# Optimization experiments

Hardware: AMD Instinct MI355X
Metric: run time of the kernel (lower is better)

## Reference

```python
import jax, jax.numpy as jnp
import numpy as np

S, B, D_MODEL, H = 2048, 2, 1024, 16
DH = D_MODEL // H
SCALE = 1.0 / np.sqrt(DH)
NEG_INF = jnp.float32(-1e30)


def setup_inputs() -> dict:
    key = jax.random.key(0)
    ks = jax.random.split(key, 12)
    std = 1.0 / np.sqrt(D_MODEL)
    inp = {
        "query": jax.random.normal(ks[0], (S, B, D_MODEL), jnp.float32),
        "key": jax.random.normal(ks[1], (S, B, D_MODEL), jnp.float32),
        "value": jax.random.normal(ks[2], (S, B, D_MODEL), jnp.float32),
        # causal mask, shape (seq_q, seq_k, 1) per prepare_mask asserts
        "mask": jnp.tril(jnp.ones((S, S), dtype=bool))[:, :, None],
        # params stored (in, out) for x @ W
        "Wq": jax.random.normal(ks[3], (D_MODEL, H * DH), jnp.float32) * std,
        "bq": jnp.zeros((H * DH,), jnp.float32),
        "Wk": jax.random.normal(ks[4], (D_MODEL, H * DH), jnp.float32) * std,
        "bk": jnp.zeros((H * DH,), jnp.float32),
        "Wv": jax.random.normal(ks[5], (D_MODEL, H * DH), jnp.float32) * std,
        "bv": jnp.zeros((H * DH,), jnp.float32),
        "Wo": jax.random.normal(ks[6], (D_MODEL, D_MODEL), jnp.float32) * std,
        "bo": jnp.zeros((D_MODEL,), jnp.float32),
    }
    return inp


def reference(query, key, value, mask, Wq, bq, Wk, bk, Wv, bv, Wo, bo):
    seq_len, batch, _ = query.shape
    # project and split heads: (S, B, H, DH)
    q = (query @ Wq + bq).reshape(seq_len, batch, H, DH)
    k = (key @ Wk + bk).reshape(key.shape[0], batch, H, DH)
    v = (value @ Wv + bv).reshape(value.shape[0], batch, H, DH)
    # scores: (seq_q, batch, heads, seq_k)
    scores = jnp.einsum("ibhd,jbhd->ibhj", q, k) * SCALE
    # mask (seq_q, seq_k, batch_or_1) -> broadcast to (seq_q, batch, 1, seq_k)
    m = jnp.transpose(mask, (0, 2, 1))[:, :, None, :]
    scores = jnp.where(m, scores, NEG_INF)
    attn = jax.nn.softmax(scores, axis=-1)  # dropout_prob=0.0 (eval)
    x = jnp.einsum("ibhj,jbhd->ibhd", attn, v)
    x = x.reshape(seq_len, batch, H * DH)
    return x @ Wo + bo
```

## Files before the change

### kernel.cpp

```cpp
#include <hip/hip_runtime.h>
#include <hip/hip_bf16.h>
#include <cstdint>

#define S_LEN 2048
#define BATCH 2
#define DM    1024
#define NH    16
#define DH    64
#define SL2E  0.18033688011112042f

typedef short s8v __attribute__((ext_vector_type(8)));
typedef float f4v __attribute__((ext_vector_type(4)));

__device__ __forceinline__ ushort f2bf(float x) {
  union { float f; uint32_t u; } v; v.f = x;
  uint32_t r = v.u + 0x7fffu + ((v.u >> 16) & 1u);
  return (ushort)(r >> 16);
}

typedef __attribute__((address_space(1))) const void gas_void;
typedef __attribute__((address_space(3))) void las_void;
__device__ __forceinline__ void gld16(void* l, const void* g) {
  __builtin_amdgcn_global_load_lds((gas_void*)(uintptr_t)g,
                                   (las_void*)(uintptr_t)l, 16, 0, 0);
}

__global__ __launch_bounds__(256)
void wtrans(const float* W0, const float* W1, const float* W2, const float* W3,
            ushort* T0, ushort* T1, ushort* T2, ushort* T3) {
  const float* W; ushort* T;
  switch (blockIdx.z) {
    case 0:  W = W0; T = T0; break;
    case 1:  W = W1; T = T1; break;
    case 2:  W = W2; T = T2; break;
    default: W = W3; T = T3; break;
  }
  __shared__ ushort tile[32][33];
  const int n0 = blockIdx.x * 32, k0 = blockIdx.y * 32;
  const int tx = threadIdx.x, ty = threadIdx.y;
  #pragma unroll
  for (int r = ty; r < 32; r += 8)
    tile[r][tx] = f2bf(W[(size_t)(k0 + r) * DM + n0 + tx]);
  __syncthreads();
  #pragma unroll
  for (int r = ty; r < 32; r += 8)
    T[(size_t)(n0 + r) * DM + k0 + tx] = tile[tx][r];
}

__global__ __launch_bounds__(256)
void castx(const float* __restrict__ X0, const float* __restrict__ X1,
           const float* __restrict__ X2,
           ushort* __restrict__ O0, ushort* __restrict__ O1,
           ushort* __restrict__ O2) {
  const float* X; ushort* O;
  switch (blockIdx.y) {
    case 0:  X = X0; O = O0; break;
    case 1:  X = X1; O = O1; break;
    default: X = X2; O = O2; break;
  }
  const size_t i = ((size_t)blockIdx.x * 256 + threadIdx.x) * 4;
  const float4 v = *(const float4*)(X + i);
  ushort4 h;
  h.x = f2bf(v.x); h.y = f2bf(v.y); h.z = f2bf(v.z); h.w = f2bf(v.w);
  *(ushort4*)(O + i) = h;
}

__global__ __launch_bounds__(256)
void gemm_qkv(const ushort* __restrict__ Xq, const ushort* __restrict__ Xk,
              const ushort* __restrict__ Xv,
              const ushort* __restrict__ Wqt, const ushort* __restrict__ Wkt,
              const ushort* __restrict__ Wvt,
              const float* __restrict__ bq, const float* __restrict__ bk,
              const float* __restrict__ bv,
              ushort* __restrict__ Qh, ushort* __restrict__ Kh,
              ushort* __restrict__ Vt) {
  const int z = blockIdx.z;
  const ushort* A    = z == 0 ? Xq  : z == 1 ? Xk  : Xv;
  const ushort* Bt   = z == 0 ? Wqt : z == 1 ? Wkt : Wvt;
  const float*  bias = z == 0 ? bq  : z == 1 ? bk  : bv;

  __shared__ __align__(16) ushort ldsA[128 * 32];
  __shared__ __align__(16) ushort ldsB[128 * 32];

  const int tid = threadIdx.x, lane = tid & 63, w = tid >> 6;
  const int wr = w >> 1, wc = w & 1;
  const int lrow = lane & 15, quad = lane >> 4;
  const int m0 = blockIdx.x * 128, n0 = blockIdx.y * 128;

  const int sr4 = lane >> 2;
  const int sc  = ((lane & 3) ^ ((lane >> 3) & 3)) * 8;

  const ushort* gA[2]; ushort* lA[2];
  const ushort* gB[2]; ushort* lB[2];
  #pragma unroll
  for (int t = 0; t < 2; t++) {
    const int c = 2 * w + t;
    gA[t] = A  + (size_t)(m0 + c * 16 + sr4) * DM + sc;
    lA[t] = &ldsA[c * 512];
    gB[t] = Bt + (size_t)(n0 + c * 16 + sr4) * DM + sc;
    lB[t] = &ldsB[c * 512];
  }

  const ushort* pa[4]; const ushort* pb[4];
  #pragma unroll
  for (int i = 0; i < 4; i++)
    pa[i] = &ldsA[(wr * 64 + i * 16 + lrow) * 32 + (quad ^ ((lrow >> 1) & 3)) * 8];
  #pragma unroll
  for (int j = 0; j < 4; j++)
    pb[j] = &ldsB[(wc * 64 + j * 16 + lrow) * 32 + (quad ^ ((lrow >> 1) & 3)) * 8];

  f4v acc[4][4];
  #pragma unroll
  for (int i = 0; i < 4; i++)
    #pragma unroll
    for (int j = 0; j < 4; j++)
      acc[i][j] = f4v{0.f, 0.f, 0.f, 0.f};

  for (int k0 = 0; k0 < DM; k0 += 32) {
    __syncthreads();
    #pragma unroll
    for (int t = 0; t < 2; t++) { gld16(lA[t], gA[t] + k0); gld16(lB[t], gB[t] + k0); }
    __syncthreads();

    s8v af[4], bf[4];
    #pragma unroll
    for (int i = 0; i < 4; i++) af[i] = *(const s8v*)pa[i];
    #pragma unroll
    for (int j = 0; j < 4; j++) bf[j] = *(const s8v*)pb[j];
    #pragma unroll
    for (int i = 0; i < 4; i++)
      #pragma unroll
      for (int j = 0; j < 4; j++)
        acc[i][j] = __builtin_amdgcn_mfma_f32_16x16x32_bf16(af[i], bf[j], acc[i][j], 0, 0, 0);
  }

  #pragma unroll
  for (int i = 0; i < 4; i++) {
    #pragma unroll
    for (int j = 0; j < 4; j++) {
      const int n = n0 + wc * 64 + j * 16 + lrow;
      const float bval = bias[n];
      const int mb = m0 + wr * 64 + i * 16 + quad * 4;
      #pragma unroll
      for (int r = 0; r < 4; r++) {
        const int m = mb + r;
        const float val = acc[i][j][r] + bval;
        const int s = m >> 1, b = m & 1;
        const int h = n >> 6, d = n & 63;
        const int bhid = b * NH + h;
        if (z <= 1) {
          ushort* O = (z == 0) ? Qh : Kh;
          O[((size_t)bhid * S_LEN + s) * DH + d] = f2bf(val);
        } else {
          Vt[((size_t)bhid * DH + d) * S_LEN + s] = f2bf(val);
        }
      }
    }
  }
}

__global__ __launch_bounds__(256)
void attn(const ushort* __restrict__ Qh, const ushort* __restrict__ Kh,
          const ushort* __restrict__ Vt, ushort* __restrict__ X) {
  __shared__ __align__(16) ushort Klds[2 * 64 * 64];
  __shared__ __align__(16) ushort Vlds[2 * 64 * 64];
  __shared__ __align__(16) ushort Plds[4 * 32 * 72];

  const int tid = threadIdx.x, lane = tid & 63, w = tid >> 6;
  const int lrow = lane & 15, quad = lane >> 4;
  const int bh = blockIdx.x;
  const int qt = (int)gridDim.y - 1 - (int)blockIdx.y;
  const int iw = qt * 128 + w * 32;
  const int nj = 2 * qt + 2;

  const int srow = lane >> 3;
  const int scol = ((lane & 7) ^ srow) * 8;
  const ushort* gK0 = Kh + ((size_t)bh * S_LEN + 2 * w * 8 + srow) * DH + scol;
  const ushort* gK1 = gK0 + 8 * DH;
  const ushort* gV0 = Vt + ((size_t)bh * DH + 2 * w * 8 + srow) * S_LEN + scol;
  const ushort* gV1 = gV0 + 8 * S_LEN;
  ushort* lK0 = &Klds[2 * w * 512]; ushort* lK1 = lK0 + 512;
  ushort* lV0 = &Vlds[2 * w * 512]; ushort* lV1 = lV0 + 512;

  s8v aq[2][2];
  #pragma unroll
  for (int is = 0; is < 2; is++)
    #pragma unroll
    for (int kk = 0; kk < 2; kk++)
      aq[is][kk] = *(const s8v*)(Qh + ((size_t)bh * S_LEN + iw + is * 16 + lrow) * DH +
                                 kk * 32 + quad * 8);

  const int f8 = lrow & 7;
  const ushort* pk[4][2]; const ushort* pv[4][2]; const ushort* pp[2][2];
  #pragma unroll
  for (int s4 = 0; s4 < 4; s4++)
    #pragma unroll
    for (int kk = 0; kk < 2; kk++) {
      pk[s4][kk] = &Klds[(s4 * 16 + lrow) * 64 + (((kk * 4 + quad) ^ f8) * 8)];
      pv[s4][kk] = &Vlds[(s4 * 16 + lrow) * 64 + (((kk * 4 + quad) ^ f8) * 8)];
    }
  #pragma unroll
  for (int is = 0; is < 2; is++)
    #pragma unroll
    for (int kk = 0; kk < 2; kk++)
      pp[is][kk] = &Plds[(w * 32 + is * 16 + lrow) * 72 + kk * 32 + quad * 8];
  ushort* pw = &Plds[w * 32 * 72];

  f4v o[2][4];
  float ls[2][4];
  #pragma unroll
  for (int is = 0; is < 2; is++) {
    #pragma unroll
    for (int d4 = 0; d4 < 4; d4++) o[is][d4] = f4v{0.f, 0.f, 0.f, 0.f};
    #pragma unroll
    for (int r = 0; r < 4; r++) ls[is][r] = 0.f;
  }

  gld16(lK0, gK0); gld16(lK1, gK1); gld16(lV0, gV0); gld16(lV1, gV1);

  for (int jt = 0; jt < nj; jt++) {
    const int j0 = jt * 64;
    __syncthreads();
    const int cur = (jt & 1) * 4096;
    if (jt + 1 < nj) {
      const int nxt = ((jt + 1) & 1) * 4096;
      const size_t jn = (size_t)(jt + 1) * 64;
      gld16(lK0 + nxt, gK0 + jn * DH);
      gld16(lK1 + nxt, gK1 + jn * DH);
      gld16(lV0 + nxt, gV0 + jn);
      gld16(lV1 + nxt, gV1 + jn);
    }
    if (j0 > iw + 31) continue;

    f4v sc[2][4];
    #pragma unroll
    for (int is = 0; is < 2; is++)
      #pragma unroll
      for (int s4 = 0; s4 < 4; s4++) sc[is][s4] = f4v{0.f, 0.f, 0.f, 0.f};
    #pragma unroll
    for (int s4 = 0; s4 < 4; s4++) {
      const s8v b0 = *(const s8v*)(pk[s4][0] + cur);
      const s8v b1 = *(const s8v*)(pk[s4][1] + cur);
      sc[0][s4] = __builtin_amdgcn_mfma_f32_16x16x32_bf16(aq[0][0], b0, sc[0][s4], 0, 0, 0);
      sc[1][s4] = __builtin_amdgcn_mfma_f32_16x16x32_bf16(aq[1][0], b0, sc[1][s4], 0, 0, 0);
      sc[0][s4] = __builtin_amdgcn_mfma_f32_16x16x32_bf16(aq[0][1], b1, sc[0][s4], 0, 0, 0);
      sc[1][s4] = __builtin_amdgcn_mfma_f32_16x16x32_bf16(aq[1][1], b1, sc[1][s4], 0, 0, 0);
    }

    const bool needmask = (j0 + 63) > iw;
    #pragma unroll
    for (int is = 0; is < 2; is++)
      #pragma unroll
      for (int s4 = 0; s4 < 4; s4++) {
        const int jg = j0 + s4 * 16 + lrow;
        #pragma unroll
        for (int r = 0; r < 4; r++) {
          float e = exp2f(sc[is][s4][r] * SL2E);
          if (needmask) {
            const int ig = iw + is * 16 + quad * 4 + r;
            e = (jg > ig) ? 0.f : e;
          }
          ls[is][r] += e;
          pw[(is * 16 + quad * 4 + r) * 72 + s4 * 16 + lrow] = f2bf(e);
        }
      }

    s8v ap[2][2];
    #pragma unroll
    for (int is = 0; is < 2; is++)
      #pragma unroll
      for (int kk = 0; kk < 2; kk++) ap[is][kk] = *(const s8v*)pp[is][kk];

    #pragma unroll
    for (int d4 = 0; d4 < 4; d4++) {
      const s8v v0 = *(const s8v*)(pv[d4][0] + cur);
      const s8v v1 = *(const s8v*)(pv[d4][1] + cur);
      o[0][d4] = __builtin_amdgcn_mfma_f32_16x16x32_bf16(ap[0][0], v0, o[0][d4], 0, 0, 0);
      o[1][d4] = __builtin_amdgcn_mfma_f32_16x16x32_bf16(ap[1][0], v0, o[1][d4], 0, 0, 0);
      o[0][d4] = __builtin_amdgcn_mfma_f32_16x16x32_bf16(ap[0][1], v1, o[0][d4], 0, 0, 0);
      o[1][d4] = __builtin_amdgcn_mfma_f32_16x16x32_bf16(ap[1][1], v1, o[1][d4], 0, 0, 0);
    }
  }

  #pragma unroll
  for (int msk = 1; msk < 16; msk <<= 1)
    #pragma unroll
    for (int is = 0; is < 2; is++)
      #pragma unroll
      for (int r = 0; r < 4; r++)
        ls[is][r] += __shfl_xor(ls[is][r], msk, 64);

  const int bb = bh >> 4, h = bh & 15;
  #pragma unroll
  for (int is = 0; is < 2; is++)
    #pragma unroll
    for (int r = 0; r < 4; r++) {
      const float inv = 1.0f / ls[is][r];
      const int ig = iw + is * 16 + quad * 4 + r;
      #pragma unroll
      for (int d4 = 0; d4 < 4; d4++)
        X[((size_t)ig * BATCH + bb) * DM + h * DH + d4 * 16 + lrow] =
            f2bf(o[is][d4][r] * inv);
    }
}

__global__ __launch_bounds__(256)
void gemm_out(const ushort* __restrict__ A, const ushort* __restrict__ Bt,
              const float* __restrict__ bias, float* __restrict__ C) {
  __shared__ __align__(16) ushort ldsA[128 * 32];
  __shared__ __align__(16) ushort ldsB[128 * 32];

  const int tid = threadIdx.x, lane = tid & 63, w = tid >> 6;
  const int wr = w >> 1, wc = w & 1;
  const int lrow = lane & 15, quad = lane >> 4;
  const int m0 = blockIdx.x * 128, n0 = blockIdx.y * 128;

  const int sr4 = lane >> 2;
  const int sc  = ((lane & 3) ^ ((lane >> 3) & 3)) * 8;

  const ushort* gA[2]; ushort* lA[2];
  const ushort* gB[2]; ushort* lB[2];
  #pragma unroll
  for (int t = 0; t < 2; t++) {
    const int c = 2 * w + t;
    gA[t] = A  + (size_t)(m0 + c * 16 + sr4) * DM + sc;
    lA[t] = &ldsA[c * 512];
    gB[t] = Bt + (size_t)(n0 + c * 16 + sr4) * DM + sc;
    lB[t] = &ldsB[c * 512];
  }

  const ushort* pa[4]; const ushort* pb[4];
  #pragma unroll
  for (int i = 0; i < 4; i++)
    pa[i] = &ldsA[(wr * 64 + i * 16 + lrow) * 32 + (quad ^ ((lrow >> 1) & 3)) * 8];
  #pragma unroll
  for (int j = 0; j < 4; j++)
    pb[j] = &ldsB[(wc * 64 + j * 16 + lrow) * 32 + (quad ^ ((lrow >> 1) & 3)) * 8];

  f4v acc[4][4];
  #pragma unroll
  for (int i = 0; i < 4; i++)
    #pragma unroll
    for (int j = 0; j < 4; j++)
      acc[i][j] = f4v{0.f, 0.f, 0.f, 0.f};

  for (int k0 = 0; k0 < DM; k0 += 32) {
    __syncthreads();
    #pragma unroll
    for (int t = 0; t < 2; t++) { gld16(lA[t], gA[t] + k0); gld16(lB[t], gB[t] + k0); }
    __syncthreads();

    s8v af[4], bf[4];
    #pragma unroll
    for (int i = 0; i < 4; i++) af[i] = *(const s8v*)pa[i];
    #pragma unroll
    for (int j = 0; j < 4; j++) bf[j] = *(const s8v*)pb[j];
    #pragma unroll
    for (int i = 0; i < 4; i++)
      #pragma unroll
      for (int j = 0; j < 4; j++)
        acc[i][j] = __builtin_amdgcn_mfma_f32_16x16x32_bf16(af[i], bf[j], acc[i][j], 0, 0, 0);
  }

  #pragma unroll
  for (int i = 0; i < 4; i++)
    #pragma unroll
    for (int j = 0; j < 4; j++) {
      const int n = n0 + wc * 64 + j * 16 + lrow;
      const float bval = bias[n];
      const int mb = m0 + wr * 64 + i * 16 + quad * 4;
      #pragma unroll
      for (int r = 0; r < 4; r++)
        C[(size_t)(mb + r) * DM + n] = acc[i][j][r] + bval;
    }
}

extern "C" void kernel_launch(void* const* d_in, const int* in_sizes, int n_in,
                              void* d_out, int out_size, void* d_ws, size_t ws_size,
                              hipStream_t stream) {
  const float* query = (const float*)d_in[0];
  const float* key_  = (const float*)d_in[1];
  const float* value = (const float*)d_in[2];
  const float* Wq = (const float*)d_in[4];
  const float* bq = (const float*)d_in[5];
  const float* Wk = (const float*)d_in[6];
  const float* bk = (const float*)d_in[7];
  const float* Wv = (const float*)d_in[8];
  const float* bv = (const float*)d_in[9];
  const float* Wo = (const float*)d_in[10];
  const float* bo = (const float*)d_in[11];

  ushort* Wqt = (ushort*)d_ws;
  ushort* Wkt = Wqt + (size_t)1024 * 1024;
  ushort* Wvt = Wkt + (size_t)1024 * 1024;
  ushort* Wot = Wvt + (size_t)1024 * 1024;
  ushort* Xbq = Wot + (size_t)1024 * 1024;
  ushort* Xbk = Xbq + (size_t)4 * 1024 * 1024;
  ushort* Xbv = Xbk + (size_t)4 * 1024 * 1024;
  ushort* Qh  = Xbv + (size_t)4 * 1024 * 1024;
  ushort* Kh  = Qh  + (size_t)4 * 1024 * 1024;
  ushort* Vt  = Kh  + (size_t)4 * 1024 * 1024;
  ushort* Xa  = Xbq;

  wtrans<<<dim3(32, 32, 4), dim3(32, 8), 0, stream>>>(Wq, Wk, Wv, Wo,
                                                      Wqt, Wkt, Wvt, Wot);
  castx<<<dim3(4096, 3), 256, 0, stream>>>(query, key_, value, Xbq, Xbk, Xbv);
  gemm_qkv<<<dim3(32, 8, 3), 256, 0, stream>>>(Xbq, Xbk, Xbv,
                                               Wqt, Wkt, Wvt, bq, bk, bv,
                                               Qh, Kh, Vt);
  attn<<<dim3(32, 16), 256, 0, stream>>>(Qh, Kh, Vt, Xa);
  gemm_out<<<dim3(32, 8), 256, 0, stream>>>(Xa, Wot, bo, (float*)d_out);
}
```

Baseline: 266.2 us.

## Split long causal attention tiles across two blocks, widen GEMM K-step, stage V transpose

```diff
diff --git a/kernel.cpp b/kernel.cpp
--- a/kernel.cpp
+++ b/kernel.cpp
@@ -16,6 +16,15 @@
   union { float f; uint32_t u; } v; v.f = x;
   uint32_t r = v.u + 0x7fffu + ((v.u >> 16) & 1u);
   return (ushort)(r >> 16);
+}
+__device__ __forceinline__ uint32_t fbits(float x) {
+  union { float f; uint32_t u; } v; v.f = x; return v.u;
+}
+__device__ __forceinline__ uint32_t bfrnd(uint32_t u) {
+  return u + 0x7fffu + ((u >> 16) & 1u);
+}
+__device__ __forceinline__ uint32_t packbf(uint32_t flo, uint32_t fhi) {
+  return __builtin_amdgcn_perm(bfrnd(fhi), bfrnd(flo), 0x07060302u);
 }
 
 typedef __attribute__((address_space(1))) const void gas_void;
@@ -79,35 +88,38 @@
   const ushort* Bt   = z == 0 ? Wqt : z == 1 ? Wkt : Wvt;
   const float*  bias = z == 0 ? bq  : z == 1 ? bk  : bv;
 
-  __shared__ __align__(16) ushort ldsA[128 * 32];
-  __shared__ __align__(16) ushort ldsB[128 * 32];
+  __shared__ __align__(16) ushort lds[20480];
+  ushort* ldsA = lds;
+  ushort* ldsB = lds + 8192;
 
   const int tid = threadIdx.x, lane = tid & 63, w = tid >> 6;
   const int wr = w >> 1, wc = w & 1;
   const int lrow = lane & 15, quad = lane >> 4;
   const int m0 = blockIdx.x * 128, n0 = blockIdx.y * 128;
 
-  const int sr4 = lane >> 2;
-  const int sc  = ((lane & 3) ^ ((lane >> 3) & 3)) * 8;
-
-  const ushort* gA[2]; ushort* lA[2];
-  const ushort* gB[2]; ushort* lB[2];
-  #pragma unroll
-  for (int t = 0; t < 2; t++) {
-    const int c = 2 * w + t;
-    gA[t] = A  + (size_t)(m0 + c * 16 + sr4) * DM + sc;
+  const int srow = lane >> 3;
+  const int scol = ((lane & 7) ^ srow) * 8;
+
+  const ushort* gA[4]; ushort* lA[4];
+  const ushort* gB[4]; ushort* lB[4];
+  #pragma unroll
+  for (int t = 0; t < 4; t++) {
+    const int c = 4 * w + t;
+    gA[t] = A  + (size_t)(m0 + c * 8 + srow) * DM + scol;
     lA[t] = &ldsA[c * 512];
-    gB[t] = Bt + (size_t)(n0 + c * 16 + sr4) * DM + sc;
+    gB[t] = Bt + (size_t)(n0 + c * 8 + srow) * DM + scol;
     lB[t] = &ldsB[c * 512];
   }
 
-  const ushort* pa[4]; const ushort* pb[4];
-  #pragma unroll
-  for (int i = 0; i < 4; i++)
-    pa[i] = &ldsA[(wr * 64 + i * 16 + lrow) * 32 + (quad ^ ((lrow >> 1) & 3)) * 8];
-  #pragma unroll
-  for (int j = 0; j < 4; j++)
-    pb[j] = &ldsB[(wc * 64 + j * 16 + lrow) * 32 + (quad ^ ((lrow >> 1) & 3)) * 8];
+  const int f8 = lrow & 7;
+  const ushort *pa[2][4], *pb[2][4];
+  #pragma unroll
+  for (int kk = 0; kk < 2; kk++)
+    #pragma unroll
+    for (int i = 0; i < 4; i++) {
+      pa[kk][i] = &ldsA[(wr * 64 + i * 16 + lrow) * 64 + (((kk * 4 + quad) ^ f8) * 8)];
+      pb[kk][i] = &ldsB[(wc * 64 + i * 16 + lrow) * 64 + (((kk * 4 + quad) ^ f8) * 8)];
+    }
 
   f4v acc[4][4];
   #pragma unroll
@@ -116,52 +128,77 @@
     for (int j = 0; j < 4; j++)
       acc[i][j] = f4v{0.f, 0.f, 0.f, 0.f};
 
-  for (int k0 = 0; k0 < DM; k0 += 32) {
+  for (int k0 = 0; k0 < DM; k0 += 64) {
     __syncthreads();
     #pragma unroll
-    for (int t = 0; t < 2; t++) { gld16(lA[t], gA[t] + k0); gld16(lB[t], gB[t] + k0); }
+    for (int t = 0; t < 4; t++) { gld16(lA[t], gA[t] + k0); gld16(lB[t], gB[t] + k0); }
     __syncthreads();
-
-    s8v af[4], bf[4];
-    #pragma unroll
-    for (int i = 0; i < 4; i++) af[i] = *(const s8v*)pa[i];
-    #pragma unroll
-    for (int j = 0; j < 4; j++) bf[j] = *(const s8v*)pb[j];
+    #pragma unroll
+    for (int kk = 0; kk < 2; kk++) {
+      s8v af[4], bf[4];
+      #pragma unroll
+      for (int i = 0; i < 4; i++) af[i] = *(const s8v*)pa[kk][i];
+      #pragma unroll
+      for (int j = 0; j < 4; j++) bf[j] = *(const s8v*)pb[kk][j];
+      #pragma unroll
+      for (int i = 0; i < 4; i++)
+        #pragma unroll
+        for (int j = 0; j < 4; j++)
+          acc[i][j] = __builtin_amdgcn_mfma_f32_16x16x32_bf16(af[i], bf[j], acc[i][j], 0, 0, 0);
+    }
+  }
+
+  if (z <= 1) {
+    ushort* O = (z == 0) ? Qh : Kh;
     #pragma unroll
     for (int i = 0; i < 4; i++)
       #pragma unroll
-      for (int j = 0; j < 4; j++)
-        acc[i][j] = __builtin_amdgcn_mfma_f32_16x16x32_bf16(af[i], bf[j], acc[i][j], 0, 0, 0);
-  }
-
-  #pragma unroll
-  for (int i = 0; i < 4; i++) {
-    #pragma unroll
-    for (int j = 0; j < 4; j++) {
-      const int n = n0 + wc * 64 + j * 16 + lrow;
-      const float bval = bias[n];
-      const int mb = m0 + wr * 64 + i * 16 + quad * 4;
-      #pragma unroll
-      for (int r = 0; r < 4; r++) {
-        const int m = mb + r;
-        const float val = acc[i][j][r] + bval;
-        const int s = m >> 1, b = m & 1;
-        const int h = n >> 6, d = n & 63;
-        const int bhid = b * NH + h;
-        if (z <= 1) {
-          ushort* O = (z == 0) ? Qh : Kh;
-          O[((size_t)bhid * S_LEN + s) * DH + d] = f2bf(val);
-        } else {
-          Vt[((size_t)bhid * DH + d) * S_LEN + s] = f2bf(val);
+      for (int j = 0; j < 4; j++) {
+        const int n = n0 + wc * 64 + j * 16 + lrow;
+        const float bval = bias[n];
+        const int mb = m0 + wr * 64 + i * 16 + quad * 4;
+        #pragma unroll
+        for (int r = 0; r < 4; r++) {
+          const int m = mb + r;
+          const int s = m >> 1, b = m & 1;
+          const int h = n >> 6, d = n & 63;
+          O[((size_t)(b * NH + h) * S_LEN + s) * DH + d] = f2bf(acc[i][j][r] + bval);
         }
       }
-    }
+  } else {
+    __syncthreads();
+    ushort* tw = lds + w * 5120;
+    #pragma unroll
+    for (int i = 0; i < 4; i++)
+      #pragma unroll
+      for (int j = 0; j < 4; j++) {
+        const int n_l = j * 16 + lrow;
+        const float bval = bias[n0 + wc * 64 + n_l];
+        const int sbase = i * 8 + quad * 2;
+        const uint32_t p0 = packbf(fbits(acc[i][j][0] + bval), fbits(acc[i][j][2] + bval));
+        const uint32_t p1 = packbf(fbits(acc[i][j][1] + bval), fbits(acc[i][j][3] + bval));
+        *(uint32_t*)&tw[n_l * 40 + sbase]        = p0;
+        *(uint32_t*)&tw[2560 + n_l * 40 + sbase] = p1;
+      }
+    const int s0 = (m0 >> 1) + wr * 32;
+    #pragma unroll
+    for (int b = 0; b < 2; b++)
+      #pragma unroll
+      for (int p = 0; p < 4; p++) {
+        const int d_l = p * 16 + (lane >> 2);
+        const int c   = lane & 3;
+        const s8v v = *(const s8v*)&tw[b * 2560 + d_l * 40 + c * 8];
+        const int n = n0 + wc * 64 + d_l;
+        const int h = n >> 6, d = n & 63;
+        *(s8v*)&Vt[((size_t)(b * NH + h) * DH + d) * S_LEN + s0 + c * 8] = v;
+      }
   }
 }
 
 __global__ __launch_bounds__(256)
 void attn(const ushort* __restrict__ Qh, const ushort* __restrict__ Kh,
-          const ushort* __restrict__ Vt, ushort* __restrict__ X) {
+          const ushort* __restrict__ Vt, ushort* __restrict__ X,
+          float* __restrict__ Opart, float* __restrict__ lpart) {
   __shared__ __align__(16) ushort Klds[2 * 64 * 64];
   __shared__ __align__(16) ushort Vlds[2 * 64 * 64];
   __shared__ __align__(16) ushort Plds[4 * 32 * 72];
@@ -169,9 +206,18 @@
   const int tid = threadIdx.x, lane = tid & 63, w = tid >> 6;
   const int lrow = lane & 15, quad = lane >> 4;
   const int bh = blockIdx.x;
-  const int qt = (int)gridDim.y - 1 - (int)blockIdx.y;
+  const int slot = blockIdx.y;
+  int qt, jlo, jhi, part;
+  if (slot < 8) { qt = slot; jlo = 0; jhi = 2 * qt + 2; part = -1; }
+  else {
+    const int s2 = slot - 8;
+    qt = 8 + (s2 >> 1);
+    const int half = s2 & 1;
+    jlo = half * (qt + 1);
+    jhi = jlo + (qt + 1);
+    part = s2;
+  }
   const int iw = qt * 128 + w * 32;
-  const int nj = 2 * qt + 2;
 
   const int srow = lane >> 3;
   const int scol = ((lane & 7) ^ srow) * 8;
@@ -216,13 +262,20 @@
     for (int r = 0; r < 4; r++) ls[is][r] = 0.f;
   }
 
-  gld16(lK0, gK0); gld16(lK1, gK1); gld16(lV0, gV0); gld16(lV1, gV1);
-
-  for (int jt = 0; jt < nj; jt++) {
+  {
+    const int b0 = (jlo & 1) * 4096;
+    const size_t j0 = (size_t)jlo * 64;
+    gld16(lK0 + b0, gK0 + j0 * DH);
+    gld16(lK1 + b0, gK1 + j0 * DH);
+    gld16(lV0 + b0, gV0 + j0);
+    gld16(lV1 + b0, gV1 + j0);
+  }
+
+  for (int jt = jlo; jt < jhi; jt++) {
     const int j0 = jt * 64;
     __syncthreads();
     const int cur = (jt & 1) * 4096;
-    if (jt + 1 < nj) {
+    if (jt + 1 < jhi) {
       const int nxt = ((jt + 1) & 1) * 4096;
       const size_t jn = (size_t)(jt + 1) * 64;
       gld16(lK0 + nxt, gK0 + jn * DH);
@@ -290,52 +343,101 @@
       for (int r = 0; r < 4; r++)
         ls[is][r] += __shfl_xor(ls[is][r], msk, 64);
 
-  const int bb = bh >> 4, h = bh & 15;
-  #pragma unroll
-  for (int is = 0; is < 2; is++)
-    #pragma unroll
-    for (int r = 0; r < 4; r++) {
-      const float inv = 1.0f / ls[is][r];
-      const int ig = iw + is * 16 + quad * 4 + r;
-      #pragma unroll
-      for (int d4 = 0; d4 < 4; d4++)
-        X[((size_t)ig * BATCH + bb) * DM + h * DH + d4 * 16 + lrow] =
-            f2bf(o[is][d4][r] * inv);
-    }
+  if (part < 0) {
+    const int bb = bh >> 4, h = bh & 15;
+    #pragma unroll
+    for (int is = 0; is < 2; is++)
+      #pragma unroll
+      for (int r = 0; r < 4; r++) {
+        const float inv = 1.0f / ls[is][r];
+        const int ig = iw + is * 16 + quad * 4 + r;
+        #pragma unroll
+        for (int d4 = 0; d4 < 4; d4++)
+          X[((size_t)ig * BATCH + bb) * DM + h * DH + d4 * 16 + lrow] =
+              f2bf(o[is][d4][r] * inv);
+      }
+  } else {
+    float* Op = Opart + ((size_t)(bh * 16 + part)) * 8192 + (size_t)w * 32 * 64;
+    #pragma unroll
+    for (int is = 0; is < 2; is++)
+      #pragma unroll
+      for (int r = 0; r < 4; r++) {
+        const int row_l = is * 16 + quad * 4 + r;
+        #pragma unroll
+        for (int d4 = 0; d4 < 4; d4++)
+          Op[row_l * 64 + d4 * 16 + lrow] = o[is][d4][r];
+      }
+    if (lrow == 0) {
+      float* lp = lpart + (size_t)(bh * 16 + part) * 128 + w * 32;
+      #pragma unroll
+      for (int is = 0; is < 2; is++)
+        #pragma unroll
+        for (int r = 0; r < 4; r++)
+          lp[is * 16 + quad * 4 + r] = ls[is][r];
+    }
+  }
+}
+
+__global__ __launch_bounds__(256)
+void combine(const float* __restrict__ Opart, const float* __restrict__ lpart,
+             ushort* __restrict__ X) {
+  const size_t gid = (size_t)blockIdx.x * 256 + threadIdx.x;
+  const int dv  = gid & 15;
+  const int row = (gid >> 4) & 127;
+  const int bh  = (gid >> 11) & 31;
+  const int qt8 = gid >> 16;
+  const int pa = qt8 * 2, pb = pa + 1;
+  const size_t ba = ((size_t)(bh * 16 + pa)) * 8192 + row * 64 + dv * 4;
+  const size_t bb_ = ((size_t)(bh * 16 + pb)) * 8192 + row * 64 + dv * 4;
+  const float4 va = *(const float4*)(Opart + ba);
+  const float4 vb = *(const float4*)(Opart + bb_);
+  const float l = lpart[(size_t)(bh * 16 + pa) * 128 + row] +
+                  lpart[(size_t)(bh * 16 + pb) * 128 + row];
+  const float inv = 1.0f / l;
+  const int qpos = (qt8 + 8) * 128 + row;
+  const int b = bh >> 4, h = bh & 15;
+  ushort4 hv;
+  hv.x = f2bf((va.x + vb.x) * inv);
+  hv.y = f2bf((va.y + vb.y) * inv);
+  hv.z = f2bf((va.z + vb.z) * inv);
+  hv.w = f2bf((va.w + vb.w) * inv);
+  *(ushort4*)&X[(((size_t)qpos * BATCH + b) * NH + h) * DH + dv * 4] = hv;
 }
 
 __global__ __launch_bounds__(256)
 void gemm_out(const ushort* __restrict__ A, const ushort* __restrict__ Bt,
               const float* __restrict__ bias, float* __restrict__ C) {
-  __shared__ __align__(16) ushort ldsA[128 * 32];
-  __shared__ __align__(16) ushort ldsB[128 * 32];
+  __shared__ __align__(16) ushort ldsA[128 * 64];
+  __shared__ __align__(16) ushort ldsB[128 * 64];
 
   const int tid = threadIdx.x, lane = tid & 63, w = tid >> 6;
   const int wr = w >> 1, wc = w & 1;
   const int lrow = lane & 15, quad = lane >> 4;
   const int m0 = blockIdx.x * 128, n0 = blockIdx.y * 128;
 
-  const int sr4 = lane >> 2;
-  const int sc  = ((lane & 3) ^ ((lane >> 3) & 3)) * 8;
-
-  const ushort* gA[2]; ushort* lA[2];
-  const ushort* gB[2]; ushort* lB[2];
-  #pragma unroll
-  for (int t = 0; t < 2; t++) {
-    const int c = 2 * w + t;
-    gA[t] = A  + (size_t)(m0 + c * 16 + sr4) * DM + sc;
+  const int srow = lane >> 3;
+  const int scol = ((lane & 7) ^ srow) * 8;
+
+  const ushort* gA[4]; ushort* lA[4];
+  const ushort* gB[4]; ushort* lB[4];
+  #pragma unroll
+  for (int t = 0; t < 4; t++) {
+    const int c = 4 * w + t;
+    gA[t] = A  + (size_t)(m0 + c * 8 + srow) * DM + scol;
     lA[t] = &ldsA[c * 512];
-    gB[t] = Bt + (size_t)(n0 + c * 16 + sr4) * DM + sc;
+    gB[t] = Bt + (size_t)(n0 + c * 8 + srow) * DM + scol;
     lB[t] = &ldsB[c * 512];
   }
 
-  const ushort* pa[4]; const ushort* pb[4];
-  #pragma unroll
-  for (int i = 0; i < 4; i++)
-    pa[i] = &ldsA[(wr * 64 + i * 16 + lrow) * 32 + (quad ^ ((lrow >> 1) & 3)) * 8];
-  #pragma unroll
-  for (int j = 0; j < 4; j++)
-    pb[j] = &ldsB[(wc * 64 + j * 16 + lrow) * 32 + (quad ^ ((lrow >> 1) & 3)) * 8];
+  const int f8 = lrow & 7;
+  const ushort *pa[2][4], *pb[2][4];
+  #pragma unroll
+  for (int kk = 0; kk < 2; kk++)
+    #pragma unroll
+    for (int i = 0; i < 4; i++) {
+      pa[kk][i] = &ldsA[(wr * 64 + i * 16 + lrow) * 64 + (((kk * 4 + quad) ^ f8) * 8)];
+      pb[kk][i] = &ldsB[(wc * 64 + i * 16 + lrow) * 64 + (((kk * 4 + quad) ^ f8) * 8)];
+    }
 
   f4v acc[4][4];
   #pragma unroll
@@ -344,22 +446,24 @@
     for (int j = 0; j < 4; j++)
       acc[i][j] = f4v{0.f, 0.f, 0.f, 0.f};
 
-  for (int k0 = 0; k0 < DM; k0 += 32) {
+  for (int k0 = 0; k0 < DM; k0 += 64) {
     __syncthreads();
     #pragma unroll
-    for (int t = 0; t < 2; t++) { gld16(lA[t], gA[t] + k0); gld16(lB[t], gB[t] + k0); }
+    for (int t = 0; t < 4; t++) { gld16(lA[t], gA[t] + k0); gld16(lB[t], gB[t] + k0); }
     __syncthreads();
-
-    s8v af[4], bf[4];
-    #pragma unroll
-    for (int i = 0; i < 4; i++) af[i] = *(const s8v*)pa[i];
-    #pragma unroll
-    for (int j = 0; j < 4; j++) bf[j] = *(const s8v*)pb[j];
-    #pragma unroll
-    for (int i = 0; i < 4; i++)
-      #pragma unroll
-      for (int j = 0; j < 4; j++)
-        acc[i][j] = __builtin_amdgcn_mfma_f32_16x16x32_bf16(af[i], bf[j], acc[i][j], 0, 0, 0);
+    #pragma unroll
+    for (int kk = 0; kk < 2; kk++) {
+      s8v af[4], bf[4];
+      #pragma unroll
+      for (int i = 0; i < 4; i++) af[i] = *(const s8v*)pa[kk][i];
+      #pragma unroll
+      for (int j = 0; j < 4; j++) bf[j] = *(const s8v*)pb[kk][j];
+      #pragma unroll
+      for (int i = 0; i < 4; i++)
+        #pragma unroll
+        for (int j = 0; j < 4; j++)
+          acc[i][j] = __builtin_amdgcn_mfma_f32_16x16x32_bf16(af[i], bf[j], acc[i][j], 0, 0, 0);
+    }
   }
 
   #pragma unroll
@@ -400,6 +504,8 @@
   ushort* Qh  = Xbv + (size_t)4 * 1024 * 1024;
   ushort* Kh  = Qh  + (size_t)4 * 1024 * 1024;
   ushort* Vt  = Kh  + (size_t)4 * 1024 * 1024;
+  float*  Opart = (float*)Xbk;
+  float*  lpart = (float*)(Vt + (size_t)4 * 1024 * 1024);
   ushort* Xa  = Xbq;
 
   wtrans<<<dim3(32, 32, 4), dim3(32, 8), 0, stream>>>(Wq, Wk, Wv, Wo,
@@ -408,6 +514,7 @@
   gemm_qkv<<<dim3(32, 8, 3), 256, 0, stream>>>(Xbq, Xbk, Xbv,
                                                Wqt, Wkt, Wvt, bq, bk, bv,
                                                Qh, Kh, Vt);
-  attn<<<dim3(32, 16), 256, 0, stream>>>(Qh, Kh, Vt, Xa);
+  attn<<<dim3(32, 24), 256, 0, stream>>>(Qh, Kh, Vt, Xa, Opart, lpart);
+  combine<<<2048, 256, 0, stream>>>(Opart, lpart, Xa);
   gemm_out<<<dim3(32, 8), 256, 0, stream>>>(Xa, Wot, bo, (float*)d_out);
 }
```

Measured after the change: 262.0 us. About the same (-1.6%).
